# Kernel optimization log

Hardware: AMD Instinct MI355X
Metric: run time of the kernel (lower is better)

The kernel has to match this reference:

```python
import jax, jax.numpy as jnp
import numpy as np

NUM_HEADS = 16

def setup_inputs() -> dict:
    key = jax.random.key(0)
    ks = jax.random.split(key, 9)
    E = 1024
    T, B = 2048, 2
    s = E ** -0.5
    return {
        "query": jax.random.normal(ks[0], (T, B, E), dtype=jnp.float32),
        "Wq": jax.random.normal(ks[1], (E, E), dtype=jnp.float32) * s,
        "bq": jax.random.normal(ks[2], (E,), dtype=jnp.float32) * 0.02,
        "Wk": jax.random.normal(ks[3], (E, E), dtype=jnp.float32) * s,
        "bk": jax.random.normal(ks[4], (E,), dtype=jnp.float32) * 0.02,
        "Wv": jax.random.normal(ks[5], (E, E), dtype=jnp.float32) * s,
        "bv": jax.random.normal(ks[6], (E,), dtype=jnp.float32) * 0.02,
        "Wo": jax.random.normal(ks[7], (E, E), dtype=jnp.float32) * s,
        "bo": jax.random.normal(ks[8], (E,), dtype=jnp.float32) * 0.02,
    }

def reference(query, Wq, bq, Wk, bk, Wv, bv, Wo, bo):
    # query: [T, B, E] (seq-first, fairseq/ESM layout)
    T, B, E = query.shape
    H = NUM_HEADS
    D = E // H
    scaling = D ** -0.5
    # projections (eqx Linear: x @ W.T + b); note k/v also come from `query` (self-attention)
    q = (query @ Wq.T + bq) * scaling
    k = query @ Wk.T + bk
    v = query @ Wv.T + bv
    # [T, B, E] -> [B*H, T, D]
    q = q.reshape(T, B * H, D).transpose(1, 0, 2)
    k = k.reshape(T, B * H, D).transpose(1, 0, 2)
    v = v.reshape(T, B * H, D).transpose(1, 0, 2)
    # full score matrix [B*H, T, T], softmax in fp32 (as in original)
    scores = jnp.einsum('ntd,nsd->nts', q, k)
    attn_w = jax.nn.softmax(scores.astype(jnp.float32), axis=-1)
    attn = jnp.einsum('nts,nsd->ntd', attn_w.astype(v.dtype), v)
    # [B*H, T, D] -> [T, B, E]
    attn = attn.transpose(1, 0, 2).reshape(T, B, E)
    return attn @ Wo.T + bo
```

## Files before the change

### kernel.cpp

```cpp
#include <hip/hip_runtime.h>
#include <hip/hip_bf16.h>


typedef __attribute__((ext_vector_type(8))) short short8;
typedef __attribute__((ext_vector_type(4))) float f32x4;
typedef __attribute__((ext_vector_type(16))) float f32x16;
typedef __attribute__((ext_vector_type(4))) unsigned u32x4;

#define T_DIM 2048
#define B_DIM 2
#define E_DIM 1024
#define H_DIM 16
#define D_DIM 64
#define M_ROWS (T_DIM * B_DIM)
#define QKV_N (3 * E_DIM)
#define HEAD_ELEMS (32 * 2048 * 64)
#define LOG2E 1.44269504088896340736f

__device__ __forceinline__ unsigned short f2bf(float f) {
    unsigned u = __builtin_bit_cast(unsigned, f);
    unsigned r = (u + 0x7fffu + ((u >> 16) & 1u)) >> 16;
    return (unsigned short)r;
}

__device__ __forceinline__ unsigned cvt_pk_bf16(float lo, float hi) {
    unsigned d;
    asm("v_cvt_pk_bf16_f32 %0, %1, %2" : "=v"(d) : "v"(lo), "v"(hi));
    return d;
}

__device__ __forceinline__ void gload_lds16(const void* g, void* l) {
    __builtin_amdgcn_global_load_lds(
        (const __attribute__((address_space(1))) void*)g,
        (__attribute__((address_space(3))) void*)l, 16, 0, 0);
}

__device__ __forceinline__ f32x16 mfma32(short8 a, short8 b, f32x16 c) {
    return __builtin_amdgcn_mfma_f32_32x32x16_bf16(a, b, c, 0, 0, 0);
}

__global__ __launch_bounds__(256) void cast_all(
    const float* __restrict__ X,
    const float* __restrict__ Wq, const float* __restrict__ Wk,
    const float* __restrict__ Wv, const float* __restrict__ Wo,
    const float* __restrict__ bq, const float* __restrict__ bk,
    const float* __restrict__ bv,
    unsigned short* __restrict__ Xbf,
    unsigned short* __restrict__ Wcat,
    unsigned short* __restrict__ Wobf,
    float* __restrict__ biasq)
{
    int idx = blockIdx.x * 256 + threadIdx.x;
    if (idx >= (1 << 20)) {
        int i = idx - (1 << 20);
        for (int j = i; j < 3072; j += 256) {
            float v;
            if (j < 1024)       v = 0.125f * LOG2E * bq[j];
            else if (j < 2048)  v = bk[j - 1024];
            else                v = bv[j - 2048];
            biasq[j] = v;
        }
        return;
    }
    size_t base = (size_t)idx * 8;
    int row = (int)(base >> 10);
    int col = (int)(base & 1023);
    const float* src;
    unsigned short* dst;
    float scale = 1.0f;
    if (row < 4096) {
        src = X + base;
        dst = Xbf + base;
    } else if (row < 7168) {
        int wrow = row - 4096;
        if (wrow < 1024)      { src = Wq + ((size_t)wrow << 10) + col; scale = 0.125f * LOG2E; }
        else if (wrow < 2048) { src = Wk + ((size_t)(wrow - 1024) << 10) + col; }
        else                  { src = Wv + ((size_t)(wrow - 2048) << 10) + col; }
        dst = Wcat + ((size_t)wrow << 10) + col;
    } else {
        int wrow = row - 7168;
        src = Wo + ((size_t)wrow << 10) + col;
        dst = Wobf + ((size_t)wrow << 10) + col;
    }
    float4 f0 = *(const float4*)src;
    float4 f1 = *(const float4*)(src + 4);
    short8 r;
    r[0] = (short)f2bf(f0.x * scale);
    r[1] = (short)f2bf(f0.y * scale);
    r[2] = (short)f2bf(f0.z * scale);
    r[3] = (short)f2bf(f0.w * scale);
    r[4] = (short)f2bf(f1.x * scale);
    r[5] = (short)f2bf(f1.y * scale);
    r[6] = (short)f2bf(f1.z * scale);
    r[7] = (short)f2bf(f1.w * scale);
    *(short8*)dst = r;
}

struct GemmCtx {
    const unsigned short* A;
    const unsigned short* B;
    int K, by, bx, wave, lane, wr, wc, lr, lg;
};

__device__ __forceinline__ void gemm_stage(
    const GemmCtx& g, unsigned short* Ast, unsigned short* Bst, int kt)
{
#pragma unroll
    for (int pass = 0; pass < 2; ++pass) {
        int c = pass * 256 + g.wave * 64 + g.lane;
        int row = c >> 2, kc = c & 3;
        gload_lds16(g.A + (size_t)(g.by * 128 + row) * g.K + kt + kc * 8,
                    (char*)Ast + c * 16);
        gload_lds16(g.B + (size_t)(g.bx * 128 + row) * g.K + kt + kc * 8,
                    (char*)Bst + c * 16);
    }
}

template <bool DO_STAGE, bool LASTWAIT>
__device__ __forceinline__ void gemm_step(
    const GemmCtx& g,
    unsigned short* Acs, unsigned short* Bcs,
    unsigned short* Ast, unsigned short* Bst, int kt_next,
    f32x4 (&acc)[4][4])
{
    if constexpr (LASTWAIT) asm volatile("s_waitcnt vmcnt(0)" ::: "memory");
    else                    asm volatile("s_waitcnt vmcnt(4)" ::: "memory");
    __builtin_amdgcn_s_barrier();
    __builtin_amdgcn_sched_barrier(0);
    if constexpr (DO_STAGE) gemm_stage(g, Ast, Bst, kt_next);

    short8 af[4], bf[4];
#pragma unroll
    for (int m = 0; m < 4; ++m)
        af[m] = *(const short8*)&Acs[(g.wr * 64 + m * 16 + g.lr) * 32 + g.lg * 8];
#pragma unroll
    for (int n = 0; n < 4; ++n)
        bf[n] = *(const short8*)&Bcs[(g.wc * 64 + n * 16 + g.lr) * 32 + g.lg * 8];
    __builtin_amdgcn_s_setprio(1);
#pragma unroll
    for (int m = 0; m < 4; ++m)
#pragma unroll
        for (int n = 0; n < 4; ++n)
            acc[m][n] = __builtin_amdgcn_mfma_f32_16x16x32_bf16(af[m], bf[n], acc[m][n], 0, 0, 0);
    __builtin_amdgcn_s_setprio(0);
}

template <int MODE>
__global__ __launch_bounds__(256) void gemm_bt(
    const unsigned short* __restrict__ A,
    const unsigned short* __restrict__ B,
    const float* __restrict__ bias,
    void* __restrict__ outp,
    int M, int N, int K)
{
    __shared__ alignas(16) unsigned short As[3][128 * 32];
    __shared__ alignas(16) unsigned short Bs[3][128 * 32];
    const int tid = threadIdx.x;
    const int wave = tid >> 6, lane = tid & 63;
    const int lr = lane & 15, lg = lane >> 4;
    const int nbx = N >> 7;
    const int bx = blockIdx.x % nbx, by = blockIdx.x / nbx;
    const int wr = wave >> 1, wc = wave & 1;

    GemmCtx g{A, B, K, by, bx, wave, lane, wr, wc, lr, lg};
    f32x4 acc[4][4] = {};

    unsigned short *A0 = &As[0][0], *A1 = &As[1][0], *A2 = &As[2][0];
    unsigned short *B0 = &Bs[0][0], *B1 = &Bs[1][0], *B2 = &Bs[2][0];

    gemm_stage(g, A0, B0, 0);
    gemm_stage(g, A1, B1, 32);
#pragma unroll 1
    for (int it = 0; it < 10; ++it) {
        int kb = it * 96;
        gemm_step<true, false>(g, A0, B0, A2, B2, kb + 64, acc);
        gemm_step<true, false>(g, A1, B1, A0, B0, kb + 96, acc);
        gemm_step<true, false>(g, A2, B2, A1, B1, kb + 128, acc);
    }
    gemm_step<false, false>(g, A0, B0, nullptr, nullptr, 0, acc);
    gemm_step<false, true >(g, A1, B1, nullptr, nullptr, 0, acc);

    const int gcol0 = bx * 128 + wc * 64;
    const int grow0 = by * 128 + wr * 64;
    if (MODE == 0) {
        unsigned short* qb = (unsigned short*)outp;
#pragma unroll
        for (int m = 0; m < 4; ++m) {
#pragma unroll
            for (int n = 0; n < 4; ++n) {
                int col = gcol0 + n * 16 + lr;
                float bsv = bias[col];
                int which = col >> 10;
                int e = col & 1023;
                int h = e >> 6, d = e & 63;
                if (which < 2) {
                    unsigned short* bufb = qb + (size_t)which * HEAD_ELEMS;
#pragma unroll
                    for (int j = 0; j < 4; ++j) {
                        int r = grow0 + m * 16 + lg * 4 + j;
                        int t = r >> 1, b = r & 1;
                        int bh = b * 16 + h;
                        bufb[((size_t)bh * 2048 + t) * 64 + d] = f2bf(acc[m][n][j] + bsv);
                    }
                } else {
                    unsigned* vT32 = (unsigned*)(qb + (size_t)2 * HEAD_ELEMS);
                    int t0 = (grow0 + m * 16 + lg * 4) >> 1;
                    int dwidx = t0 >> 1;
                    int dwp = (dwidx & ~6) | ((dwidx & 2) << 1) | ((dwidx & 4) >> 1);
                    unsigned w0 = (unsigned)f2bf(acc[m][n][0] + bsv) |
                                  ((unsigned)f2bf(acc[m][n][2] + bsv) << 16);
                    unsigned w1 = (unsigned)f2bf(acc[m][n][1] + bsv) |
                                  ((unsigned)f2bf(acc[m][n][3] + bsv) << 16);
                    vT32[(size_t)(h * 64 + d) * 1024 + dwp] = w0;
                    vT32[(size_t)((16 + h) * 64 + d) * 1024 + dwp] = w1;
                }
            }
        }
    } else {
        float* O = (float*)outp;
#pragma unroll
        for (int m = 0; m < 4; ++m) {
#pragma unroll
            for (int n = 0; n < 4; ++n) {
                int col = gcol0 + n * 16 + lr;
                float bsv = bias[col];
#pragma unroll
                for (int j = 0; j < 4; ++j) {
                    int r = grow0 + m * 16 + lg * 4 + j;
                    O[(size_t)r * N + col] = acc[m][n][j] + bsv;
                }
            }
        }
    }
}

struct AttnCtx {
    const unsigned short* kh;
    const unsigned short* vh;
    int tid, ql, hi;
};

__device__ __forceinline__ void attn_stage(
    const AttnCtx& cx, char* Kst, char* Vst, int kt)
{
#pragma unroll
    for (int p = 0; p < 2; ++p) {
        int c = p * 256 + cx.tid;
        int row = c >> 3;
        int sxb = ((c & 7) * 16) ^ ((row & 7) << 4);
        gload_lds16(cx.kh + (size_t)(kt + row) * 64 + (sxb >> 1), Kst + c * 16);
    }
#pragma unroll
    for (int p = 0; p < 2; ++p) {
        int c = p * 256 + cx.tid;
        int d = c >> 3;
        int sxb = ((c & 7) * 16) ^ ((d & 7) << 4);
        gload_lds16(cx.vh + (size_t)d * 2048 + kt + (sxb >> 1), Vst + c * 16);
    }
}

template<bool DO_PV, bool DO_STAGE, bool LASTWAIT>
__device__ __forceinline__ void attn_step(
    const AttnCtx& cx, int kt_next,
    const char* Kb, const char* Vprv, char* Kst, char* Vst,
    const short8 (&qv)[4],
    const short8 (&paP)[4], short8 (&paC)[4],
    f32x16 (&accO)[2], float& lrun)
{
    const int ql = cx.ql, hi = cx.hi;
    if constexpr (LASTWAIT) asm volatile("s_waitcnt vmcnt(0)" ::: "memory");
    else                    asm volatile("s_waitcnt vmcnt(4)" ::: "memory");
    __builtin_amdgcn_s_barrier();
    __builtin_amdgcn_sched_barrier(0);

    if constexpr (DO_STAGE) attn_stage(cx, Kst, Vst, kt_next);

    f32x16 st[2] = {};
    __builtin_amdgcn_s_setprio(1);
#pragma unroll
    for (int m = 0; m < 2; ++m) {
        int krow = m * 32 + ql;
#pragma unroll
        for (int c = 0; c < 4; ++c) {
            int bo = (krow * 128 + c * 32 + hi * 16) ^ ((krow & 7) << 4);
            short8 ka = *(const short8*)(Kb + bo);
            st[m] = mfma32(ka, qv[c], st[m]);
        }
    }
    if constexpr (DO_PV) {
#pragma unroll
        for (int n = 0; n < 2; ++n) {
            int d = n * 32 + ql;
#pragma unroll
            for (int kc = 0; kc < 4; ++kc) {
                int bo = (d * 128 + kc * 32 + hi * 16) ^ ((d & 7) << 4);
                short8 va = *(const short8*)(Vprv + bo);
                accO[n] = mfma32(va, paP[kc], accO[n]);
            }
        }
    }
    __builtin_amdgcn_s_setprio(0);
    __builtin_amdgcn_sched_barrier(0);

    float rs0 = 0.f, rs1 = 0.f, rs2 = 0.f, rs3 = 0.f;
#pragma unroll
    for (int m = 0; m < 2; ++m) {
#pragma unroll
        for (int r = 0; r < 16; r += 4) {
            float e0 = __builtin_amdgcn_exp2f(st[m][r + 0]);
            float e1 = __builtin_amdgcn_exp2f(st[m][r + 1]);
            float e2 = __builtin_amdgcn_exp2f(st[m][r + 2]);
            float e3 = __builtin_amdgcn_exp2f(st[m][r + 3]);
            st[m][r + 0] = e0; st[m][r + 1] = e1;
            st[m][r + 2] = e2; st[m][r + 3] = e3;
            rs0 += e0; rs1 += e1; rs2 += e2; rs3 += e3;
        }
    }
    lrun += (rs0 + rs1) + (rs2 + rs3);

#pragma unroll
    for (int kc = 0; kc < 4; ++kc) {
        int m = kc >> 1, b8 = (kc & 1) * 8;
        u32x4 u;
        u[0] = cvt_pk_bf16(st[m][b8 + 0], st[m][b8 + 1]);
        u[1] = cvt_pk_bf16(st[m][b8 + 2], st[m][b8 + 3]);
        u[2] = cvt_pk_bf16(st[m][b8 + 4], st[m][b8 + 5]);
        u[3] = cvt_pk_bf16(st[m][b8 + 6], st[m][b8 + 7]);
        paC[kc] = __builtin_bit_cast(short8, u);
    }
}

__global__ __launch_bounds__(256, 2) void attn_fwd(
    const unsigned short* __restrict__ q,
    const unsigned short* __restrict__ k,
    const unsigned short* __restrict__ vT,
    unsigned short* __restrict__ outb)
{
    __shared__ alignas(16) unsigned short Ks[4][64 * 64];
    __shared__ alignas(16) unsigned short Vs[4][64 * 64];
    const int tid = threadIdx.x, wv = tid >> 6, l = tid & 63;
    const int ql = l & 31, hi = l >> 5;
    const int lid = blockIdx.x;
    const int xcd = lid & 7, slot = lid >> 3;
    const int bh = xcd * 4 + (slot >> 4);
    const int q0 = (slot & 15) * 128;
    const unsigned short* qh = q + (size_t)bh * (2048 * 64);
    AttnCtx cx;
    cx.kh = k + (size_t)bh * (2048 * 64);
    cx.vh = vT + (size_t)bh * (64 * 2048);
    cx.tid = tid; cx.ql = ql; cx.hi = hi;

    char* K0 = (char*)&Ks[0][0]; char* K1 = (char*)&Ks[1][0];
    char* K2 = (char*)&Ks[2][0]; char* K3 = (char*)&Ks[3][0];
    char* V0 = (char*)&Vs[0][0]; char* V1 = (char*)&Vs[1][0];
    char* V2 = (char*)&Vs[2][0]; char* V3 = (char*)&Vs[3][0];

    const int qrow = q0 + wv * 32 + ql;
    short8 qv[4];
#pragma unroll
    for (int c = 0; c < 4; ++c)
        qv[c] = *(const short8*)&qh[(size_t)qrow * 64 + c * 16 + hi * 8];

    f32x16 accO[2] = {};
    float lrun = 0.0f;
    short8 paA[4], paB[4];

    attn_stage(cx, K0, V0, 0);
    attn_stage(cx, K1, V1, 64);

    attn_step<false, true, false>(cx, 2 * 64, K0, nullptr, K2, V2,
                                  qv, paB, paA, accO, lrun);
    attn_step<true, true, false>(cx, 3 * 64, K1, V0, K3, V3,
                                 qv, paA, paB, accO, lrun);
#pragma unroll 1
    for (int it = 0; it < 7; ++it) {
        const int t = 2 + it * 4;
        attn_step<true, true, false>(cx, (t + 2) * 64, K2, V1, K0, V0,
                                     qv, paB, paA, accO, lrun);
        attn_step<true, true, false>(cx, (t + 3) * 64, K3, V2, K1, V1,
                                     qv, paA, paB, accO, lrun);
        attn_step<true, true, false>(cx, (t + 4) * 64, K0, V3, K2, V2,
                                     qv, paB, paA, accO, lrun);
        attn_step<true, true, false>(cx, (t + 5) * 64, K1, V0, K3, V3,
                                     qv, paA, paB, accO, lrun);
    }
    attn_step<true, false, false>(cx, 0, K2, V1, nullptr, nullptr,
                                  qv, paB, paA, accO, lrun);
    attn_step<true, false, true>(cx, 0, K3, V2, nullptr, nullptr,
                                 qv, paA, paB, accO, lrun);
#pragma unroll
    for (int n = 0; n < 2; ++n) {
        int d = n * 32 + ql;
#pragma unroll
        for (int kc = 0; kc < 4; ++kc) {
            int bo = (d * 128 + kc * 32 + hi * 16) ^ ((d & 7) << 4);
            short8 va = *(const short8*)(V3 + bo);
            accO[n] = mfma32(va, paB[kc], accO[n]);
        }
    }

    const float ltot = lrun + __shfl_xor(lrun, 32);
    const float inv = 1.0f / ltot;
    const int b = bh >> 4, h = bh & 15;
    const int orow = qrow * 2 + b;
#pragma unroll
    for (int n = 0; n < 2; ++n)
#pragma unroll
        for (int rq = 0; rq < 4; ++rq) {
            uint2 u;
            u.x = cvt_pk_bf16(accO[n][rq * 4 + 0] * inv, accO[n][rq * 4 + 1] * inv);
            u.y = cvt_pk_bf16(accO[n][rq * 4 + 2] * inv, accO[n][rq * 4 + 3] * inv);
            *(uint2*)&outb[(size_t)orow * 1024 + h * 64 + n * 32 + rq * 8 + hi * 4] = u;
        }
}

extern "C" void kernel_launch(void* const* d_in, const int* in_sizes, int n_in,
                              void* d_out, int out_size, void* d_ws, size_t ws_size,
                              hipStream_t stream) {
    const float* X  = (const float*)d_in[0];
    const float* Wq = (const float*)d_in[1];
    const float* bq = (const float*)d_in[2];
    const float* Wk = (const float*)d_in[3];
    const float* bk = (const float*)d_in[4];
    const float* Wv = (const float*)d_in[5];
    const float* bv = (const float*)d_in[6];
    const float* Wo = (const float*)d_in[7];
    const float* bo = (const float*)d_in[8];
    float* out = (float*)d_out;

    char* ws = (char*)d_ws;
    if (ws_size < ((size_t)49 << 20)) return;
    unsigned short* Xbf   = (unsigned short*)(ws);
    unsigned short* Wcat  = (unsigned short*)(ws + ((size_t)8  << 20));
    unsigned short* Wobf  = (unsigned short*)(ws + ((size_t)14 << 20));
    unsigned short* qb    = (unsigned short*)(ws + ((size_t)16 << 20));
    unsigned short* ab    = (unsigned short*)(ws + ((size_t)40 << 20));
    float*          biasq = (float*)(ws + ((size_t)48 << 20));
    unsigned short* kb  = qb + (size_t)HEAD_ELEMS;
    unsigned short* vTb = qb + (size_t)2 * HEAD_ELEMS;

    cast_all<<<4097, 256, 0, stream>>>(X, Wq, Wk, Wv, Wo, bq, bk, bv,
                                       Xbf, Wcat, Wobf, biasq);
    gemm_bt<0><<<dim3((M_ROWS / 128) * (QKV_N / 128)), 256, 0, stream>>>(
        Xbf, Wcat, biasq, (void*)qb, M_ROWS, QKV_N, E_DIM);
    attn_fwd<<<dim3(32 * 16), 256, 0, stream>>>(qb, kb, vTb, ab);
    gemm_bt<1><<<dim3((M_ROWS / 128) * (E_DIM / 128)), 256, 0, stream>>>(
        ab, Wobf, bo, (void*)out, M_ROWS, E_DIM, E_DIM);
}
```

Baseline: 115.8 us.

## Use 256x256 tiled QKV GEMM with swizzled LDS and block remapping

Replaces the 128x128 QKV projection GEMM with a dedicated 512-thread kernel that computes 256x256 output tiles. It uses K-steps of 64, double-buffered LDS with an XOR swizzle, and a blockIdx remap to group tiles. Larger tiles raise arithmetic intensity and cut global reloads of A and B. The cost is 128KB of LDS per block, more registers, and only 192 blocks, which could leave some CUs idle on a 256-CU part.

After: 123.5 us. 6.7% more time.

```diff
diff --git a/kernel.cpp b/kernel.cpp
--- a/kernel.cpp
+++ b/kernel.cpp
@@ -96,6 +96,114 @@
     *(short8*)dst = r;
 }
 
+__global__ __launch_bounds__(512, 2) void gemm256_qkv(
+    const unsigned short* __restrict__ A,
+    const unsigned short* __restrict__ B,
+    const float* __restrict__ bias,
+    unsigned short* __restrict__ qb)
+{
+    __shared__ alignas(16) unsigned short As[2][256 * 64];
+    __shared__ alignas(16) unsigned short Bs[2][256 * 64];
+    const int tid = threadIdx.x;
+    const int wave = tid >> 6, lane = tid & 63;
+    const int lr = lane & 15, lg = lane >> 4;
+    const int wr = wave >> 2, wc = wave & 3;
+    const int bid = blockIdx.x;
+    const int nb = (bid & 7) * 24 + (bid >> 3);
+    const int bx = nb % 12, by = nb / 12;
+
+    f32x4 acc[8][4] = {};
+
+    auto stage = [&](int slot, int kt) {
+#pragma unroll
+        for (int i = 0; i < 4; ++i) {
+            int c = i * 512 + tid;
+            int row = c >> 3;
+            int sxb = ((c & 7) * 16) ^ ((row & 7) << 4);
+            gload_lds16(A + (size_t)(by * 256 + row) * 1024 + kt + (sxb >> 1),
+                        (char*)&As[slot][0] + c * 16);
+        }
+#pragma unroll
+        for (int i = 0; i < 4; ++i) {
+            int c = i * 512 + tid;
+            int row = c >> 3;
+            int sxb = ((c & 7) * 16) ^ ((row & 7) << 4);
+            gload_lds16(B + (size_t)(bx * 256 + row) * 1024 + kt + (sxb >> 1),
+                        (char*)&Bs[slot][0] + c * 16);
+        }
+    };
+
+    stage(0, 0);
+#pragma unroll 1
+    for (int t = 0; t < 16; ++t) {
+        asm volatile("s_waitcnt vmcnt(0)" ::: "memory");
+        __builtin_amdgcn_s_barrier();
+        __builtin_amdgcn_sched_barrier(0);
+        if (t < 15) stage((t + 1) & 1, (t + 1) * 64);
+
+        const char* Ab = (const char*)&As[t & 1][0];
+        const char* Bb = (const char*)&Bs[t & 1][0];
+#pragma unroll
+        for (int kc = 0; kc < 2; ++kc) {
+            short8 af[8], bf[4];
+#pragma unroll
+            for (int m = 0; m < 8; ++m) {
+                int row = wr * 128 + m * 16 + lr;
+                int bo = (row * 128 + kc * 64 + lg * 16) ^ ((row & 7) << 4);
+                af[m] = *(const short8*)(Ab + bo);
+            }
+#pragma unroll
+            for (int n = 0; n < 4; ++n) {
+                int row = wc * 64 + n * 16 + lr;
+                int bo = (row * 128 + kc * 64 + lg * 16) ^ ((row & 7) << 4);
+                bf[n] = *(const short8*)(Bb + bo);
+            }
+            __builtin_amdgcn_s_setprio(1);
+#pragma unroll
+            for (int m = 0; m < 8; ++m)
+#pragma unroll
+                for (int n = 0; n < 4; ++n)
+                    acc[m][n] = __builtin_amdgcn_mfma_f32_16x16x32_bf16(af[m], bf[n], acc[m][n], 0, 0, 0);
+            __builtin_amdgcn_s_setprio(0);
+        }
+    }
+
+    const int gcol0 = bx * 256 + wc * 64;
+    const int grow0 = by * 256 + wr * 128;
+#pragma unroll
+    for (int m = 0; m < 8; ++m) {
+#pragma unroll
+        for (int n = 0; n < 4; ++n) {
+            int col = gcol0 + n * 16 + lr;
+            float bsv = bias[col];
+            int which = col >> 10;
+            int e = col & 1023;
+            int h = e >> 6, d = e & 63;
+            if (which < 2) {
+                unsigned short* bufb = qb + (size_t)which * HEAD_ELEMS;
+#pragma unroll
+                for (int j = 0; j < 4; ++j) {
+                    int r = grow0 + m * 16 + lg * 4 + j;
+                    int t = r >> 1, b = r & 1;
+                    int bh = b * 16 + h;
+                    bufb[((size_t)bh * 2048 + t) * 64 + d] = f2bf(acc[m][n][j] + bsv);
+                }
+            } else {
+                unsigned* vT32 = (unsigned*)(qb + (size_t)2 * HEAD_ELEMS);
+                int t0 = (grow0 + m * 16 + lg * 4) >> 1;
+                int dwidx = t0 >> 1;
+                int dwp = (dwidx & ~6) | ((dwidx & 2) << 1) | ((dwidx & 4) >> 1);
+                unsigned w0 = (unsigned)f2bf(acc[m][n][0] + bsv) |
+                              ((unsigned)f2bf(acc[m][n][2] + bsv) << 16);
+                unsigned w1 = (unsigned)f2bf(acc[m][n][1] + bsv) |
+                              ((unsigned)f2bf(acc[m][n][3] + bsv) << 16);
+                vT32[(size_t)(h * 64 + d) * 1024 + dwp] = w0;
+                vT32[(size_t)((16 + h) * 64 + d) * 1024 + dwp] = w1;
+            }
+        }
+    }
+}
+
 struct GemmCtx {
     const unsigned short* A;
     const unsigned short* B;
@@ -145,12 +253,11 @@
     __builtin_amdgcn_s_setprio(0);
 }
 
-template <int MODE>
-__global__ __launch_bounds__(256) void gemm_bt(
+__global__ __launch_bounds__(256) void gemm_out(
     const unsigned short* __restrict__ A,
     const unsigned short* __restrict__ B,
     const float* __restrict__ bias,
-    void* __restrict__ outp,
+    float* __restrict__ O,
     int M, int N, int K)
 {
     __shared__ alignas(16) unsigned short As[3][128 * 32];
@@ -182,53 +289,16 @@
 
     const int gcol0 = bx * 128 + wc * 64;
     const int grow0 = by * 128 + wr * 64;
-    if (MODE == 0) {
-        unsigned short* qb = (unsigned short*)outp;
-#pragma unroll
-        for (int m = 0; m < 4; ++m) {
-#pragma unroll
-            for (int n = 0; n < 4; ++n) {
-                int col = gcol0 + n * 16 + lr;
-                float bsv = bias[col];
-                int which = col >> 10;
-                int e = col & 1023;
-                int h = e >> 6, d = e & 63;
-                if (which < 2) {
-                    unsigned short* bufb = qb + (size_t)which * HEAD_ELEMS;
-#pragma unroll
-                    for (int j = 0; j < 4; ++j) {
-                        int r = grow0 + m * 16 + lg * 4 + j;
-                        int t = r >> 1, b = r & 1;
-                        int bh = b * 16 + h;
-                        bufb[((size_t)bh * 2048 + t) * 64 + d] = f2bf(acc[m][n][j] + bsv);
-                    }
-                } else {
-                    unsigned* vT32 = (unsigned*)(qb + (size_t)2 * HEAD_ELEMS);
-                    int t0 = (grow0 + m * 16 + lg * 4) >> 1;
-                    int dwidx = t0 >> 1;
-                    int dwp = (dwidx & ~6) | ((dwidx & 2) << 1) | ((dwidx & 4) >> 1);
-                    unsigned w0 = (unsigned)f2bf(acc[m][n][0] + bsv) |
-                                  ((unsigned)f2bf(acc[m][n][2] + bsv) << 16);
-                    unsigned w1 = (unsigned)f2bf(acc[m][n][1] + bsv) |
-                                  ((unsigned)f2bf(acc[m][n][3] + bsv) << 16);
-                    vT32[(size_t)(h * 64 + d) * 1024 + dwp] = w0;
-                    vT32[(size_t)((16 + h) * 64 + d) * 1024 + dwp] = w1;
-                }
-            }
-        }
-    } else {
-        float* O = (float*)outp;
-#pragma unroll
-        for (int m = 0; m < 4; ++m) {
-#pragma unroll
-            for (int n = 0; n < 4; ++n) {
-                int col = gcol0 + n * 16 + lr;
-                float bsv = bias[col];
-#pragma unroll
-                for (int j = 0; j < 4; ++j) {
-                    int r = grow0 + m * 16 + lg * 4 + j;
-                    O[(size_t)r * N + col] = acc[m][n][j] + bsv;
-                }
+#pragma unroll
+    for (int m = 0; m < 4; ++m) {
+#pragma unroll
+        for (int n = 0; n < 4; ++n) {
+            int col = gcol0 + n * 16 + lr;
+            float bsv = bias[col];
+#pragma unroll
+            for (int j = 0; j < 4; ++j) {
+                int r = grow0 + m * 16 + lg * 4 + j;
+                O[(size_t)r * N + col] = acc[m][n][j] + bsv;
             }
         }
     }
@@ -441,9 +511,8 @@
 
     cast_all<<<4097, 256, 0, stream>>>(X, Wq, Wk, Wv, Wo, bq, bk, bv,
                                        Xbf, Wcat, Wobf, biasq);
-    gemm_bt<0><<<dim3((M_ROWS / 128) * (QKV_N / 128)), 256, 0, stream>>>(
-        Xbf, Wcat, biasq, (void*)qb, M_ROWS, QKV_N, E_DIM);
+    gemm256_qkv<<<192, 512, 0, stream>>>(Xbf, Wcat, biasq, qb);
     attn_fwd<<<dim3(32 * 16), 256, 0, stream>>>(qb, kb, vTb, ab);
-    gemm_bt<1><<<dim3((M_ROWS / 128) * (E_DIM / 128)), 256, 0, stream>>>(
-        ab, Wobf, bo, (void*)out, M_ROWS, E_DIM, E_DIM);
-}
+    gemm_out<<<dim3(256), 256, 0, stream>>>(ab, Wobf, bo, out,
+                                            M_ROWS, E_DIM, E_DIM);
+}
```
